# Kernel optimization log

Measured on AMD Instinct MI355X. Metric: run time of the kernel, lower is better.

## Reference

```python
import jax, jax.numpy as jnp
import numpy as np

N = 20000
E = 320000
H = 16
C = 16
NUM_GRAPHS = 64
NEG_SLOPE = 0.2


def _gat(x, edge_index, W, a_src, a_dst, bias):
    # PyG GATConv, concat=True, shared lin for src/dst, eval mode (no dropout)
    h = (x @ W).reshape(-1, H, C)                       # [N,H,C]
    src, dst = edge_index[0], edge_index[1]
    alpha_src = jnp.sum(h * a_src, axis=-1)             # [N,H]
    alpha_dst = jnp.sum(h * a_dst, axis=-1)             # [N,H]
    alpha = alpha_src[src] + alpha_dst[dst]             # [E,H]
    alpha = jax.nn.leaky_relu(alpha, NEG_SLOPE)
    amax = jax.ops.segment_max(alpha, dst, num_segments=N)
    ex = jnp.exp(alpha - amax[dst])
    denom = jax.ops.segment_sum(ex, dst, num_segments=N)
    attn = ex / jnp.where(denom == 0, 1.0, denom)[dst]  # [E,H]
    msg = h[src] * attn[:, :, None]                     # [E,H,C]
    out = jax.ops.segment_sum(msg, dst, num_segments=N) # [N,H,C]
    return out.reshape(-1, H * C) + bias


def setup_inputs() -> dict:
    key = jax.random.key(0)
    ks = jax.random.split(key, 32)
    d = {}
    d['x'] = jax.random.normal(ks[0], (N, 20), dtype=jnp.float32)
    d['edge_index_ipv6'] = jax.random.randint(ks[1], (2, E), 0, N)
    d['edge_attr_ipv6'] = jax.random.normal(ks[2], (E, 19), dtype=jnp.float32)
    d['edge_index_tsch'] = jax.random.randint(ks[3], (2, E), 0, N)
    d['edge_attr_tsch'] = jax.random.normal(ks[4], (E, 7), dtype=jnp.float32)
    d['batch'] = jnp.sort(jax.random.randint(ks[5], (N,), 0, NUM_GRAPHS))
    s = 0.1
    d['W_i'] = jax.random.normal(ks[6], (20, H * C), dtype=jnp.float32) * s
    d['a_src_i'] = jax.random.normal(ks[7], (H, C), dtype=jnp.float32) * s
    d['a_dst_i'] = jax.random.normal(ks[8], (H, C), dtype=jnp.float32) * s
    d['b_i'] = jnp.zeros((H * C,), dtype=jnp.float32)
    d['W_t'] = jax.random.normal(ks[9], (20, H * C), dtype=jnp.float32) * s
    d['a_src_t'] = jax.random.normal(ks[10], (H, C), dtype=jnp.float32) * s
    d['a_dst_t'] = jax.random.normal(ks[11], (H, C), dtype=jnp.float32) * s
    d['b_t'] = jnp.zeros((H * C,), dtype=jnp.float32)
    d['Wf'] = jax.random.normal(ks[12], (512, 64), dtype=jnp.float32) * s
    d['bf'] = jnp.zeros((64,), dtype=jnp.float32)
    d['W1'] = jax.random.normal(ks[13], (64, 32), dtype=jnp.float32) * s
    d['b1'] = jnp.zeros((32,), dtype=jnp.float32)
    d['W2'] = jax.random.normal(ks[14], (32, 16), dtype=jnp.float32) * s
    d['b2'] = jnp.zeros((16,), dtype=jnp.float32)
    d['W3'] = jax.random.normal(ks[15], (16, 16), dtype=jnp.float32) * s
    d['b3'] = jnp.zeros((16,), dtype=jnp.float32)
    d['Wce'] = jax.random.normal(ks[16], (16, 3), dtype=jnp.float32) * s
    d['bce'] = jnp.zeros((3,), dtype=jnp.float32)
    d['Wcv'] = jax.random.normal(ks[17], (16, 3), dtype=jnp.float32) * s
    d['bcv'] = jnp.zeros((3,), dtype=jnp.float32)
    return d


def reference(x, edge_index_ipv6, edge_attr_ipv6, edge_index_tsch, edge_attr_tsch,
              batch, W_i, a_src_i, a_dst_i, b_i, W_t, a_src_t, a_dst_t, b_t,
              Wf, bf, W1, b1, W2, b2, W3, b3, Wce, bce, Wcv, bcv):
    # edge_attr_* are ignored by GATConv (edge_dim=None in PyG), as in original
    n_ipv6 = _gat(x, edge_index_ipv6, W_i, a_src_i, a_dst_i, b_i)
    n_tsch = _gat(x, edge_index_tsch, W_t, a_src_t, a_dst_t, b_t)
    h = jnp.concatenate([n_ipv6, n_tsch], axis=-1)      # [N,512]
    h = jax.nn.relu(h @ Wf + bf)
    h = jax.nn.relu(h @ W1 + b1)
    h = jax.nn.relu(h @ W2 + b2)
    h = jax.nn.relu(h @ W3 + b3)                        # [N,16]
    ssum = jax.ops.segment_sum(h, batch, num_segments=NUM_GRAPHS)
    cnt = jax.ops.segment_sum(jnp.ones((h.shape[0], 1), h.dtype), batch,
                              num_segments=NUM_GRAPHS)
    g = ssum / jnp.where(cnt == 0, 1.0, cnt)            # [G,16]
    out_event = g @ Wce + bce
    out_env = g @ Wcv + bcv
    return out_event, out_env
```

## Files before the change

### kernel.cpp

```cpp
#include <hip/hip_runtime.h>
#include <math.h>

#define N_NODES 20000
#define N_EDGES 320000
#define NG 64
#define NEG 0.2f
#define NCHUNK ((N_NODES + 255) / 256)
#define FLAGBIT (1 << 30)

typedef __attribute__((ext_vector_type(8))) short bf16x8;
typedef __attribute__((ext_vector_type(4))) float f32x4;

__device__ __forceinline__ unsigned short f2bf(float f) {
  unsigned int u = __float_as_uint(f);
  return (unsigned short)((u + 0x7fffu + ((u >> 16) & 1u)) >> 16);
}
__device__ __forceinline__ unsigned int pk2bf(float a, float b) {
  return (unsigned int)f2bf(a) | ((unsigned int)f2bf(b) << 16);
}

__global__ __launch_bounds__(256) void k_front(
    const float* __restrict__ x,
    const float* __restrict__ W_i, const float* __restrict__ as_i, const float* __restrict__ ad_i,
    const float* __restrict__ W_t, const float* __restrict__ as_t, const float* __restrict__ ad_t,
    const float* __restrict__ Wf, const float* __restrict__ bf,
    const float* __restrict__ b_i, const float* __restrict__ b_t,
    const int* __restrict__ ei0, const int* __restrict__ ei1,
    unsigned short* __restrict__ wbigfrag, float* __restrict__ bfold,
    unsigned short* __restrict__ xpadbf,
    float* __restrict__ asrc0, float* __restrict__ adst0,
    float* __restrict__ asrc1, float* __restrict__ adst1,
    int* __restrict__ fill0, int* __restrict__ fill1) {
  __shared__ float bred[4][64];
  __shared__ float xs[16][20];
  __shared__ float ws[20][64];
  int b = blockIdx.x, t = threadIdx.x;
  if (b < 160) {
    int idx = b * 256 + t;
    int ct = idx / 10240, rem = idx % 10240;
    int lane = (rem >> 3) & 63, j = rem & 7, ks = rem >> 9;
    int k = ks * 32 + ((lane >> 4) << 3) + j;
    int nc = ct * 16 + (lane & 15);
    int g = (k >= 320) ? 1 : 0;
    int r = k - g * 320;
    int ch = r >> 4, h = r & 15;
    float v = 0.f;
    if (ch < 20) {
      const float* W = g ? W_t : W_i;
      const float* wr = W + ch * 256 + (h << 4);
      const float* wf = Wf + ((g << 8) + (h << 4)) * 64 + nc;
#pragma unroll
      for (int m = 0; m < 16; ++m) v = fmaf(wr[m], wf[m * 64], v);
    }
    wbigfrag[idx] = f2bf(v);
    return;
  }
  if (b == 160) {
    int wv = t >> 6, j = t & 63;
    float p = 0.f;
    int i0 = wv * 128;
#pragma unroll 4
    for (int i = i0; i < i0 + 128; ++i) {
      float bb = (i < 256) ? b_i[i] : b_t[i - 256];
      p = fmaf(bb, Wf[i * 64 + j], p);
    }
    bred[wv][j] = p;
    __syncthreads();
    if (wv == 0) bfold[j] = bred[0][j] + bred[1][j] + bred[2][j] + bred[3][j] + bf[j];
    return;
  }
  int a = b - 161;
  int e = a * 256 + t;
  int d0 = ei0[N_EDGES + e];
  int d1 = ei1[N_EDGES + e];
  atomicAdd(&fill0[d0], 1);
  atomicAdd(&fill1[d1], 1);
  int n0 = a * 16;
  for (int i = t; i < 320; i += 256) {
    int nd = i / 20, k = i % 20;
    xs[nd][k] = x[(n0 + nd) * 20 + k];
  }
  for (int i = t; i < 1280; i += 256) {
    int k = i >> 6, c = i & 63;
    int set = c >> 5, role = (c >> 4) & 1, h = c & 15;
    const float* W = set ? W_t : W_i;
    const float* av = set ? (role ? ad_t : as_t) : (role ? ad_i : as_i);
    float v = 0.f;
#pragma unroll
    for (int j = 0; j < 16; ++j) v = fmaf(W[k * 256 + h * 16 + j], av[h * 16 + j], v);
    ws[k][c] = v;
  }
  __syncthreads();
  for (int i = t; i < 512; i += 256) {
    int nd = i >> 5, j = i & 31;
    float v = (j < 20) ? xs[nd][j] : (j == 20 ? 1.f : 0.f);
    xpadbf[(size_t)(n0 + nd) * 32 + j] = f2bf(v);
  }
#pragma unroll
  for (int i = 0; i < 4; ++i) {
    int wi = i * 256 + t;
    int nd = wi >> 6, c = wi & 63;
    float v = 0.f;
#pragma unroll
    for (int k = 0; k < 20; ++k) v = fmaf(xs[nd][k], ws[k][c], v);
    int n = n0 + nd, h = c & 15;
    float* arr = (c >> 5) ? ((c >> 4) & 1 ? adst1 : asrc1)
                          : ((c >> 4) & 1 ? adst0 : asrc0);
    arr[n * 16 + h] = v;
  }
}

__global__ __launch_bounds__(256) void k_scan(
    int* __restrict__ fill0, int* __restrict__ fill1,
    int* __restrict__ rp0, int* __restrict__ rp1,
    int* __restrict__ aggs) {
  int chunk = blockIdx.x, set = blockIdx.y;
  int* fill = set ? fill1 : fill0;
  int* rp = set ? rp1 : rp0;
  int t = threadIdx.x, lane = t & 63, wv = t >> 6;
  int i = chunk * 256 + t;
  int v = (i < N_NODES) ? fill[i] : 0;
  int s = v;
#pragma unroll
  for (int d = 1; d < 64; d <<= 1) {
    int o = __shfl_up(s, d);
    if (lane >= d) s += o;
  }
  __shared__ int wsum[4];
  if (lane == 63) wsum[wv] = s;
  __syncthreads();
  int pre = 0;
#pragma unroll
  for (int j = 0; j < 4; ++j)
    if (j < wv) pre += wsum[j];
  s += pre;
  int agg = wsum[0] + wsum[1] + wsum[2] + wsum[3];
  if (t == 0)
    __hip_atomic_store(&aggs[set * 128 + chunk], agg | FLAGBIT,
                       __ATOMIC_RELEASE, __HIP_MEMORY_SCOPE_AGENT);
  __shared__ int reds[256];
  int part = 0;
  for (int j = t; j < chunk; j += 256) {
    int a;
    do {
      a = __hip_atomic_load(&aggs[set * 128 + j], __ATOMIC_ACQUIRE,
                            __HIP_MEMORY_SCOPE_AGENT);
    } while (!(a & FLAGBIT));
    part += a & (FLAGBIT - 1);
  }
  reds[t] = part;
  __syncthreads();
  for (int st = 128; st > 0; st >>= 1) {
    if (t < st) reds[t] += reds[t + st];
    __syncthreads();
  }
  int carry = reds[0];
  int excl = carry + s - v;
  if (i < N_NODES) {
    rp[i] = excl;
    fill[i] = excl;
    if (i == N_NODES - 1) rp[N_NODES] = excl + v;
  }
}

__global__ void k_scatter(const int* __restrict__ ei0, const int* __restrict__ ei1,
                          int* __restrict__ fill0, int* __restrict__ fill1,
                          unsigned short* __restrict__ srcs0,
                          unsigned short* __restrict__ srcs1) {
  int e = blockIdx.x * blockDim.x + threadIdx.x;
  if (e >= N_EDGES) return;
  const int* ei = blockIdx.y ? ei1 : ei0;
  int* fill = blockIdx.y ? fill1 : fill0;
  unsigned short* srcs = blockIdx.y ? srcs1 : srcs0;
  int d = ei[N_EDGES + e];
  int pos = atomicAdd(&fill[d], 1);
  srcs[pos] = (unsigned short)ei[e];
}

__global__ __launch_bounds__(256) void k_gat(
    const unsigned short* __restrict__ xpadbf,
    const float* __restrict__ asrc0, const float* __restrict__ adst0,
    const float* __restrict__ asrc1, const float* __restrict__ adst1,
    const int* __restrict__ rp0, const unsigned short* __restrict__ srcs0,
    const int* __restrict__ rp1, const unsigned short* __restrict__ srcs1,
    unsigned short* __restrict__ xagg) {
  __shared__ unsigned short exsh[4][16][40];
  __shared__ unsigned short xtsh[4][2][16][40];
  int w4 = threadIdx.x >> 6, lane = threadIdx.x & 63;
  int n = blockIdx.x * 2 + (w4 >> 1);
  int g = w4 & 1;
  int eid = lane & 15, slot = lane >> 4;
  unsigned short (*ext)[40] = exsh[w4];
  unsigned short (*xtw)[16][40] = xtsh[w4];
  const float* asrc = g ? asrc1 : asrc0;
  const float* adst = g ? adst1 : adst0;
  const int* rp = g ? rp1 : rp0;
  const unsigned short* srcs = g ? srcs1 : srcs0;
  int k0 = rp[n], k1 = rp[n + 1];
  const float4 adn4 = *(const float4*)&adst[n * 16 + slot * 4];
  f32x4 acc0 = {0.f, 0.f, 0.f, 0.f}, acc1 = acc0;
  int h16 = lane & 15, e8 = (lane >> 4) * 8;
  for (int base = k0; base < k1; base += 32) {
    int e0 = base + 2 * eid, e1 = e0 + 1;
    int sa = (int)srcs[min(e0, k1 - 1)];
    int sbb = (int)srcs[min(e1, k1 - 1)];
    const float4 ava = *(const float4*)&asrc[sa * 16 + slot * 4];
    const float4 avb = *(const float4*)&asrc[sbb * 16 + slot * 4];
    const uint4 xra = *(const uint4*)&xpadbf[(size_t)sa * 32 + slot * 8];
    const uint4 xrb = *(const uint4*)&xpadbf[(size_t)sbb * 32 + slot * 8];
    float ea[4], eb[4];
    {
      float a;
      bool v0 = e0 < k1, v1 = e1 < k1;
      a = ava.x + adn4.x; a = a >= 0.f ? a : NEG * a; ea[0] = v0 ? __expf(a) : 0.f;
      a = ava.y + adn4.y; a = a >= 0.f ? a : NEG * a; ea[1] = v0 ? __expf(a) : 0.f;
      a = ava.z + adn4.z; a = a >= 0.f ? a : NEG * a; ea[2] = v0 ? __expf(a) : 0.f;
      a = ava.w + adn4.w; a = a >= 0.f ? a : NEG * a; ea[3] = v0 ? __expf(a) : 0.f;
      a = avb.x + adn4.x; a = a >= 0.f ? a : NEG * a; eb[0] = v1 ? __expf(a) : 0.f;
      a = avb.y + adn4.y; a = a >= 0.f ? a : NEG * a; eb[1] = v1 ? __expf(a) : 0.f;
      a = avb.z + adn4.z; a = a >= 0.f ? a : NEG * a; eb[2] = v1 ? __expf(a) : 0.f;
      a = avb.w + adn4.w; a = a >= 0.f ? a : NEG * a; eb[3] = v1 ? __expf(a) : 0.f;
    }
#pragma unroll
    for (int r = 0; r < 4; ++r)
      *(unsigned int*)&ext[slot * 4 + r][2 * eid] = pk2bf(ea[r], eb[r]);
    unsigned int ua[4] = {xra.x, xra.y, xra.z, xra.w};
    unsigned int ub[4] = {xrb.x, xrb.y, xrb.z, xrb.w};
#pragma unroll
    for (int q = 0; q < 8; ++q) {
      unsigned int baq = (q & 1) ? (ua[q >> 1] >> 16) : (ua[q >> 1] & 0xffffu);
      unsigned int bbq = (q & 1) ? (ub[q >> 1] >> 16) : (ub[q >> 1] & 0xffffu);
      int ch = slot * 8 + q;
      *(unsigned int*)&xtw[ch >> 4][ch & 15][2 * eid] = baq | (bbq << 16);
    }
    bf16x8 A = *(const bf16x8*)&ext[h16][e8];
    bf16x8 B0 = *(const bf16x8*)&xtw[0][h16][e8];
    bf16x8 B1 = *(const bf16x8*)&xtw[1][h16][e8];
    acc0 = __builtin_amdgcn_mfma_f32_16x16x32_bf16(A, B0, acc0, 0, 0, 0);
    acc1 = __builtin_amdgcn_mfma_f32_16x16x32_bf16(A, B1, acc1, 0, 0, 0);
  }
  float inv[4];
#pragma unroll
  for (int r = 0; r < 4; ++r) {
    float dr = __shfl(acc1[r], (lane & 48) | 4);
    inv[r] = dr > 0.f ? 1.f / dr : 0.f;
  }
  int s = lane >> 4, c = lane & 15;
  size_t nb = (size_t)n * 640 + g * 320;
  uint2 o0;
  o0.x = pk2bf(acc0[0] * inv[0], acc0[1] * inv[1]);
  o0.y = pk2bf(acc0[2] * inv[2], acc0[3] * inv[3]);
  *(uint2*)&xagg[nb + c * 16 + s * 4] = o0;
  if (c < 4) {
    uint2 o1;
    o1.x = pk2bf(acc1[0] * inv[0], acc1[1] * inv[1]);
    o1.y = pk2bf(acc1[2] * inv[2], acc1[3] * inv[3]);
    *(uint2*)&xagg[nb + 256 + c * 16 + s * 4] = o1;
  }
}

__global__ __launch_bounds__(256) void k_mlp(
    const unsigned short* __restrict__ xagg, const unsigned short* __restrict__ wbigfrag,
    const float* __restrict__ bfold,
    const float* __restrict__ W1m, const float* __restrict__ b1v,
    const float* __restrict__ W2m, const float* __restrict__ b2v,
    const float* __restrict__ W3m, const float* __restrict__ b3v,
    const int* __restrict__ batch,
    float* __restrict__ gsum, int* __restrict__ gcnt) {
  int t = threadIdx.x, w = t >> 6, lane = t & 63;
  int n0 = blockIdx.x * 16;
  __shared__ float o1[16][68];
  __shared__ float o2[16][36];
  __shared__ float o3[16][20];
  __shared__ float o4[16][17];
  __shared__ int bs[16];
  if (t < 16) bs[t] = batch[n0 + t];

  {
    int m = lane & 15, kb = lane >> 4;
    const unsigned short* aptr = xagg + (size_t)(n0 + m) * 640 + kb * 8;
    const unsigned short* bbase = wbigfrag + (size_t)w * 10240 + lane * 8;
    f32x4 acc = {0.f, 0.f, 0.f, 0.f};
#pragma unroll 5
    for (int ks = 0; ks < 20; ++ks) {
      bf16x8 af = *(const bf16x8*)(aptr + ks * 32);
      bf16x8 bfr = *(const bf16x8*)(bbase + (size_t)ks * 512);
      acc = __builtin_amdgcn_mfma_f32_16x16x32_bf16(af, bfr, acc, 0, 0, 0);
    }
    int col = lane & 15, rg = lane >> 4;
#pragma unroll
    for (int r = 0; r < 4; ++r) {
      int row = rg * 4 + r;
      o1[row][w * 16 + col] = fmaxf(acc[r] + bfold[w * 16 + col], 0.f);
    }
  }
  __syncthreads();
  int nd = t >> 4, js = t & 15;
  {
    float a0 = b1v[js], a1 = b1v[js + 16];
#pragma unroll 8
    for (int k = 0; k < 64; ++k) {
      float hv = o1[nd][k];
      a0 = fmaf(hv, W1m[k * 32 + js], a0);
      a1 = fmaf(hv, W1m[k * 32 + js + 16], a1);
    }
    o2[nd][js] = fmaxf(a0, 0.f);
    o2[nd][js + 16] = fmaxf(a1, 0.f);
  }
  __syncthreads();
  {
    float a = b2v[js];
#pragma unroll
    for (int k = 0; k < 32; ++k) a = fmaf(o2[nd][k], W2m[k * 16 + js], a);
    o3[nd][js] = fmaxf(a, 0.f);
  }
  __syncthreads();
  {
    float a = b3v[js];
#pragma unroll
    for (int k = 0; k < 16; ++k) a = fmaf(o3[nd][k], W3m[k * 16 + js], a);
    o4[nd][js] = fmaxf(a, 0.f);
  }
  __syncthreads();
  if (t < 128) {
    int s = t >> 4, jx = t & 15;
    int b = bs[0] + s;
    if (b <= bs[15]) {
      float sum = 0.f; int c = 0;
#pragma unroll
      for (int ndd = 0; ndd < 16; ++ndd)
        if (bs[ndd] == b) { sum += o4[ndd][jx]; ++c; }
      if (c > 0) {
        atomicAdd(&gsum[b * 16 + jx], sum);
        if (jx == 0) atomicAdd(&gcnt[b], c);
      }
    }
  }
}

__global__ void k_head(const float* __restrict__ gsum, const int* __restrict__ gcnt,
                       const float* __restrict__ Wce, const float* __restrict__ bce,
                       const float* __restrict__ Wcv, const float* __restrict__ bcv,
                       float* __restrict__ out) {
  int t = threadIdx.x;
  if (t >= 384) return;
  int half = t / 192, idx = t % 192;
  int b = idx / 3, r = idx % 3;
  float cnt = (float)gcnt[b];
  float inv = cnt > 0.f ? 1.f / cnt : 1.f;
  const float* Wc = half ? Wcv : Wce;
  const float* bc = half ? bcv : bce;
  float v = bc[r];
#pragma unroll
  for (int j = 0; j < 16; ++j) v = fmaf(gsum[b * 16 + j] * inv, Wc[j * 3 + r], v);
  out[t] = v;
}

extern "C" void kernel_launch(void* const* d_in, const int* in_sizes, int n_in,
                              void* d_out, int out_size, void* d_ws, size_t ws_size,
                              hipStream_t stream) {
  const float* x = (const float*)d_in[0];
  const int* ei_i = (const int*)d_in[1];
  const int* ei_t = (const int*)d_in[3];
  const int* batch = (const int*)d_in[5];
  const float* W_i = (const float*)d_in[6];
  const float* as_i = (const float*)d_in[7];
  const float* ad_i = (const float*)d_in[8];
  const float* b_i = (const float*)d_in[9];
  const float* W_t = (const float*)d_in[10];
  const float* as_t = (const float*)d_in[11];
  const float* ad_t = (const float*)d_in[12];
  const float* b_t = (const float*)d_in[13];
  const float* Wf = (const float*)d_in[14];
  const float* bf = (const float*)d_in[15];
  const float* W1 = (const float*)d_in[16];
  const float* b1 = (const float*)d_in[17];
  const float* W2 = (const float*)d_in[18];
  const float* b2 = (const float*)d_in[19];
  const float* W3 = (const float*)d_in[20];
  const float* b3 = (const float*)d_in[21];
  const float* Wce = (const float*)d_in[22];
  const float* bce = (const float*)d_in[23];
  const float* Wcv = (const float*)d_in[24];
  const float* bcv = (const float*)d_in[25];

  char* ws = (char*)d_ws;
  size_t off = 0;
  auto take = [&](size_t bytes) {
    void* p = ws + off;
    off = (off + bytes + 255) & ~(size_t)255;
    return p;
  };
  unsigned short* xpadbf = (unsigned short*)take((size_t)N_NODES * 32 * 2);
  unsigned short* xagg = (unsigned short*)take((size_t)N_NODES * 640 * 2);
  unsigned short* wbigfrag = (unsigned short*)take((size_t)40960 * 2);
  float* bfold = (float*)take((size_t)64 * 4);
  float* asrc_i = (float*)take((size_t)N_NODES * 16 * 4);
  float* adst_i = (float*)take((size_t)N_NODES * 16 * 4);
  float* asrc_t = (float*)take((size_t)N_NODES * 16 * 4);
  float* adst_t = (float*)take((size_t)N_NODES * 16 * 4);
  int* rowptr_i = (int*)take((size_t)(N_NODES + 1) * 4);
  int* rowptr_t = (int*)take((size_t)(N_NODES + 1) * 4);
  int* fill_i = (int*)take((size_t)2 * N_NODES * 4);
  int* fill_t = fill_i + N_NODES;
  unsigned short* srcs_i = (unsigned short*)take((size_t)N_EDGES * 2);
  unsigned short* srcs_t = (unsigned short*)take((size_t)N_EDGES * 2);
  float* gsum = (float*)take((size_t)(NG * 16 + NG + 256) * 4);
  int* gcnt = (int*)(gsum + NG * 16);
  int* csums = gcnt + NG;

  hipMemsetAsync(fill_i, 0, (size_t)2 * N_NODES * 4, stream);
  hipMemsetAsync(gsum, 0, (size_t)(NG * 16 + NG + 256) * 4, stream);

  k_front<<<1411, 256, 0, stream>>>(x, W_i, as_i, ad_i, W_t, as_t, ad_t,
                                    Wf, bf, b_i, b_t, ei_i, ei_t,
                                    wbigfrag, bfold, xpadbf,
                                    asrc_i, adst_i, asrc_t, adst_t,
                                    fill_i, fill_t);

  dim3 sgrid(NCHUNK, 2);
  k_scan<<<sgrid, 256, 0, stream>>>(fill_i, fill_t, rowptr_i, rowptr_t, csums);

  dim3 egrid((N_EDGES + 255) / 256, 2);
  k_scatter<<<egrid, 256, 0, stream>>>(ei_i, ei_t, fill_i, fill_t, srcs_i, srcs_t);

  k_gat<<<N_NODES / 2, 256, 0, stream>>>(xpadbf, asrc_i, adst_i, asrc_t, adst_t,
                                         rowptr_i, srcs_i, rowptr_t, srcs_t,
                                         xagg);

  k_mlp<<<N_NODES / 16, 256, 0, stream>>>(xagg, wbigfrag, bfold,
                                          W1, b1, W2, b2, W3, b3,
                                          batch, gsum, gcnt);

  k_head<<<1, 384, 0, stream>>>(gsum, gcnt, Wce, bce, Wcv, bcv, (float*)d_out);
}
```

Baseline: 137.8 us.

## Fuse GAT aggregation and MLP into one kernel, merge memsets

Merges the GAT aggregation kernel and the MLP/pooling kernel into a single kernel where each block aggregates 16 nodes (8 iterations of 2 nodes per wave pair) and then runs the MLP on those same nodes, reusing shared memory through a union buffer. The xagg rows are written and then re-read by the same block, which should mostly hit in cache, and one kernel launch is removed. The two memsets are merged into one by placing the fill and gsum buffers next to each other. In exchange, the grid shrinks from 10000 to 1250 blocks, so per-block degree imbalance is serialized within a block and there is less parallelism for hiding gather latency.

Measured after the change: 133.6 us. 1.03x faster.

```diff
diff --git a/kernel.cpp b/kernel.cpp
--- a/kernel.cpp
+++ b/kernel.cpp
@@ -177,162 +177,167 @@
   srcs[pos] = (unsigned short)ei[e];
 }
 
-__global__ __launch_bounds__(256) void k_gat(
+__global__ __launch_bounds__(256) void k_gatmlp(
     const unsigned short* __restrict__ xpadbf,
     const float* __restrict__ asrc0, const float* __restrict__ adst0,
     const float* __restrict__ asrc1, const float* __restrict__ adst1,
     const int* __restrict__ rp0, const unsigned short* __restrict__ srcs0,
     const int* __restrict__ rp1, const unsigned short* __restrict__ srcs1,
-    unsigned short* __restrict__ xagg) {
-  __shared__ unsigned short exsh[4][16][40];
-  __shared__ unsigned short xtsh[4][2][16][40];
-  int w4 = threadIdx.x >> 6, lane = threadIdx.x & 63;
-  int n = blockIdx.x * 2 + (w4 >> 1);
-  int g = w4 & 1;
-  int eid = lane & 15, slot = lane >> 4;
-  unsigned short (*ext)[40] = exsh[w4];
-  unsigned short (*xtw)[16][40] = xtsh[w4];
-  const float* asrc = g ? asrc1 : asrc0;
-  const float* adst = g ? adst1 : adst0;
-  const int* rp = g ? rp1 : rp0;
-  const unsigned short* srcs = g ? srcs1 : srcs0;
-  int k0 = rp[n], k1 = rp[n + 1];
-  const float4 adn4 = *(const float4*)&adst[n * 16 + slot * 4];
-  f32x4 acc0 = {0.f, 0.f, 0.f, 0.f}, acc1 = acc0;
-  int h16 = lane & 15, e8 = (lane >> 4) * 8;
-  for (int base = k0; base < k1; base += 32) {
-    int e0 = base + 2 * eid, e1 = e0 + 1;
-    int sa = (int)srcs[min(e0, k1 - 1)];
-    int sbb = (int)srcs[min(e1, k1 - 1)];
-    const float4 ava = *(const float4*)&asrc[sa * 16 + slot * 4];
-    const float4 avb = *(const float4*)&asrc[sbb * 16 + slot * 4];
-    const uint4 xra = *(const uint4*)&xpadbf[(size_t)sa * 32 + slot * 8];
-    const uint4 xrb = *(const uint4*)&xpadbf[(size_t)sbb * 32 + slot * 8];
-    float ea[4], eb[4];
-    {
-      float a;
-      bool v0 = e0 < k1, v1 = e1 < k1;
-      a = ava.x + adn4.x; a = a >= 0.f ? a : NEG * a; ea[0] = v0 ? __expf(a) : 0.f;
-      a = ava.y + adn4.y; a = a >= 0.f ? a : NEG * a; ea[1] = v0 ? __expf(a) : 0.f;
-      a = ava.z + adn4.z; a = a >= 0.f ? a : NEG * a; ea[2] = v0 ? __expf(a) : 0.f;
-      a = ava.w + adn4.w; a = a >= 0.f ? a : NEG * a; ea[3] = v0 ? __expf(a) : 0.f;
-      a = avb.x + adn4.x; a = a >= 0.f ? a : NEG * a; eb[0] = v1 ? __expf(a) : 0.f;
-      a = avb.y + adn4.y; a = a >= 0.f ? a : NEG * a; eb[1] = v1 ? __expf(a) : 0.f;
-      a = avb.z + adn4.z; a = a >= 0.f ? a : NEG * a; eb[2] = v1 ? __expf(a) : 0.f;
-      a = avb.w + adn4.w; a = a >= 0.f ? a : NEG * a; eb[3] = v1 ? __expf(a) : 0.f;
-    }
-#pragma unroll
-    for (int r = 0; r < 4; ++r)
-      *(unsigned int*)&ext[slot * 4 + r][2 * eid] = pk2bf(ea[r], eb[r]);
-    unsigned int ua[4] = {xra.x, xra.y, xra.z, xra.w};
-    unsigned int ub[4] = {xrb.x, xrb.y, xrb.z, xrb.w};
-#pragma unroll
-    for (int q = 0; q < 8; ++q) {
-      unsigned int baq = (q & 1) ? (ua[q >> 1] >> 16) : (ua[q >> 1] & 0xffffu);
-      unsigned int bbq = (q & 1) ? (ub[q >> 1] >> 16) : (ub[q >> 1] & 0xffffu);
-      int ch = slot * 8 + q;
-      *(unsigned int*)&xtw[ch >> 4][ch & 15][2 * eid] = baq | (bbq << 16);
-    }
-    bf16x8 A = *(const bf16x8*)&ext[h16][e8];
-    bf16x8 B0 = *(const bf16x8*)&xtw[0][h16][e8];
-    bf16x8 B1 = *(const bf16x8*)&xtw[1][h16][e8];
-    acc0 = __builtin_amdgcn_mfma_f32_16x16x32_bf16(A, B0, acc0, 0, 0, 0);
-    acc1 = __builtin_amdgcn_mfma_f32_16x16x32_bf16(A, B1, acc1, 0, 0, 0);
-  }
-  float inv[4];
-#pragma unroll
-  for (int r = 0; r < 4; ++r) {
-    float dr = __shfl(acc1[r], (lane & 48) | 4);
-    inv[r] = dr > 0.f ? 1.f / dr : 0.f;
-  }
-  int s = lane >> 4, c = lane & 15;
-  size_t nb = (size_t)n * 640 + g * 320;
-  uint2 o0;
-  o0.x = pk2bf(acc0[0] * inv[0], acc0[1] * inv[1]);
-  o0.y = pk2bf(acc0[2] * inv[2], acc0[3] * inv[3]);
-  *(uint2*)&xagg[nb + c * 16 + s * 4] = o0;
-  if (c < 4) {
-    uint2 o1;
-    o1.x = pk2bf(acc1[0] * inv[0], acc1[1] * inv[1]);
-    o1.y = pk2bf(acc1[2] * inv[2], acc1[3] * inv[3]);
-    *(uint2*)&xagg[nb + 256 + c * 16 + s * 4] = o1;
-  }
-}
-
-__global__ __launch_bounds__(256) void k_mlp(
-    const unsigned short* __restrict__ xagg, const unsigned short* __restrict__ wbigfrag,
+    unsigned short* __restrict__ xagg, const unsigned short* __restrict__ wbigfrag,
     const float* __restrict__ bfold,
     const float* __restrict__ W1m, const float* __restrict__ b1v,
     const float* __restrict__ W2m, const float* __restrict__ b2v,
     const float* __restrict__ W3m, const float* __restrict__ b3v,
     const int* __restrict__ batch,
     float* __restrict__ gsum, int* __restrict__ gcnt) {
-  int t = threadIdx.x, w = t >> 6, lane = t & 63;
+  __shared__ __align__(16) char smem_[15360];
+  int t = threadIdx.x;
+  int w4 = t >> 6, lane = t & 63;
   int n0 = blockIdx.x * 16;
-  __shared__ float o1[16][68];
-  __shared__ float o2[16][36];
-  __shared__ float o3[16][20];
-  __shared__ float o4[16][17];
-  __shared__ int bs[16];
-  if (t < 16) bs[t] = batch[n0 + t];
 
   {
-    int m = lane & 15, kb = lane >> 4;
-    const unsigned short* aptr = xagg + (size_t)(n0 + m) * 640 + kb * 8;
-    const unsigned short* bbase = wbigfrag + (size_t)w * 10240 + lane * 8;
-    f32x4 acc = {0.f, 0.f, 0.f, 0.f};
+    int eid = lane & 15, slot = lane >> 4;
+    int h16 = lane & 15, e8 = (lane >> 4) * 8;
+    unsigned short* ext = (unsigned short*)smem_ + w4 * 640;
+    unsigned short* xtw = (unsigned short*)(smem_ + 5120) + w4 * 1280;
+    int g = w4 & 1;
+    const float* asrc = g ? asrc1 : asrc0;
+    const float* adst = g ? adst1 : adst0;
+    const int* rp = g ? rp1 : rp0;
+    const unsigned short* srcs = g ? srcs1 : srcs0;
+    for (int it = 0; it < 8; ++it) {
+      int n = n0 + it * 2 + (w4 >> 1);
+      int k0 = rp[n], k1 = rp[n + 1];
+      const float4 adn4 = *(const float4*)&adst[n * 16 + slot * 4];
+      f32x4 acc0 = {0.f, 0.f, 0.f, 0.f}, acc1 = acc0;
+      for (int base = k0; base < k1; base += 32) {
+        int e0 = base + 2 * eid, e1 = e0 + 1;
+        int sa = (int)srcs[min(e0, k1 - 1)];
+        int sbb = (int)srcs[min(e1, k1 - 1)];
+        const float4 ava = *(const float4*)&asrc[sa * 16 + slot * 4];
+        const float4 avb = *(const float4*)&asrc[sbb * 16 + slot * 4];
+        const uint4 xra = *(const uint4*)&xpadbf[(size_t)sa * 32 + slot * 8];
+        const uint4 xrb = *(const uint4*)&xpadbf[(size_t)sbb * 32 + slot * 8];
+        float ea[4], eb[4];
+        {
+          float a;
+          bool v0 = e0 < k1, v1 = e1 < k1;
+          a = ava.x + adn4.x; a = a >= 0.f ? a : NEG * a; ea[0] = v0 ? __expf(a) : 0.f;
+          a = ava.y + adn4.y; a = a >= 0.f ? a : NEG * a; ea[1] = v0 ? __expf(a) : 0.f;
+          a = ava.z + adn4.z; a = a >= 0.f ? a : NEG * a; ea[2] = v0 ? __expf(a) : 0.f;
+          a = ava.w + adn4.w; a = a >= 0.f ? a : NEG * a; ea[3] = v0 ? __expf(a) : 0.f;
+          a = avb.x + adn4.x; a = a >= 0.f ? a : NEG * a; eb[0] = v1 ? __expf(a) : 0.f;
+          a = avb.y + adn4.y; a = a >= 0.f ? a : NEG * a; eb[1] = v1 ? __expf(a) : 0.f;
+          a = avb.z + adn4.z; a = a >= 0.f ? a : NEG * a; eb[2] = v1 ? __expf(a) : 0.f;
+          a = avb.w + adn4.w; a = a >= 0.f ? a : NEG * a; eb[3] = v1 ? __expf(a) : 0.f;
+        }
+#pragma unroll
+        for (int r = 0; r < 4; ++r)
+          *(unsigned int*)&ext[(slot * 4 + r) * 40 + 2 * eid] = pk2bf(ea[r], eb[r]);
+        unsigned int ua[4] = {xra.x, xra.y, xra.z, xra.w};
+        unsigned int ub[4] = {xrb.x, xrb.y, xrb.z, xrb.w};
+#pragma unroll
+        for (int q = 0; q < 8; ++q) {
+          unsigned int baq = (q & 1) ? (ua[q >> 1] >> 16) : (ua[q >> 1] & 0xffffu);
+          unsigned int bbq = (q & 1) ? (ub[q >> 1] >> 16) : (ub[q >> 1] & 0xffffu);
+          int ch = slot * 8 + q;
+          *(unsigned int*)&xtw[(ch >> 4) * 640 + (ch & 15) * 40 + 2 * eid] =
+              baq | (bbq << 16);
+        }
+        bf16x8 A = *(const bf16x8*)&ext[h16 * 40 + e8];
+        bf16x8 B0 = *(const bf16x8*)&xtw[h16 * 40 + e8];
+        bf16x8 B1 = *(const bf16x8*)&xtw[640 + h16 * 40 + e8];
+        acc0 = __builtin_amdgcn_mfma_f32_16x16x32_bf16(A, B0, acc0, 0, 0, 0);
+        acc1 = __builtin_amdgcn_mfma_f32_16x16x32_bf16(A, B1, acc1, 0, 0, 0);
+      }
+      float inv[4];
+#pragma unroll
+      for (int r = 0; r < 4; ++r) {
+        float dr = __shfl(acc1[r], (lane & 48) | 4);
+        inv[r] = dr > 0.f ? 1.f / dr : 0.f;
+      }
+      int ss = lane >> 4, c = lane & 15;
+      size_t nb = (size_t)n * 640 + g * 320;
+      uint2 o0;
+      o0.x = pk2bf(acc0[0] * inv[0], acc0[1] * inv[1]);
+      o0.y = pk2bf(acc0[2] * inv[2], acc0[3] * inv[3]);
+      *(uint2*)&xagg[nb + c * 16 + ss * 4] = o0;
+      if (c < 4) {
+        uint2 o1v;
+        o1v.x = pk2bf(acc1[0] * inv[0], acc1[1] * inv[1]);
+        o1v.y = pk2bf(acc1[2] * inv[2], acc1[3] * inv[3]);
+        *(uint2*)&xagg[nb + 256 + c * 16 + ss * 4] = o1v;
+      }
+    }
+  }
+  __syncthreads();
+
+  {
+    float* o1 = (float*)smem_;
+    float* o2 = o1 + 1088;
+    float* o3 = o2 + 576;
+    float* o4 = o3 + 320;
+    int* bs = (int*)(o4 + 272);
+    if (t < 16) bs[t] = batch[n0 + t];
+    int w = w4;
+    {
+      int m = lane & 15, kb = lane >> 4;
+      const unsigned short* aptr = xagg + (size_t)(n0 + m) * 640 + kb * 8;
+      const unsigned short* bbase = wbigfrag + (size_t)w * 10240 + lane * 8;
+      f32x4 acc = {0.f, 0.f, 0.f, 0.f};
 #pragma unroll 5
-    for (int ks = 0; ks < 20; ++ks) {
-      bf16x8 af = *(const bf16x8*)(aptr + ks * 32);
-      bf16x8 bfr = *(const bf16x8*)(bbase + (size_t)ks * 512);
-      acc = __builtin_amdgcn_mfma_f32_16x16x32_bf16(af, bfr, acc, 0, 0, 0);
-    }
-    int col = lane & 15, rg = lane >> 4;
-#pragma unroll
-    for (int r = 0; r < 4; ++r) {
-      int row = rg * 4 + r;
-      o1[row][w * 16 + col] = fmaxf(acc[r] + bfold[w * 16 + col], 0.f);
-    }
-  }
-  __syncthreads();
-  int nd = t >> 4, js = t & 15;
-  {
-    float a0 = b1v[js], a1 = b1v[js + 16];
+      for (int ks = 0; ks < 20; ++ks) {
+        bf16x8 af = *(const bf16x8*)(aptr + ks * 32);
+        bf16x8 bfr = *(const bf16x8*)(bbase + (size_t)ks * 512);
+        acc = __builtin_amdgcn_mfma_f32_16x16x32_bf16(af, bfr, acc, 0, 0, 0);
+      }
+      int col = lane & 15, rg = lane >> 4;
+#pragma unroll
+      for (int r = 0; r < 4; ++r) {
+        int row = rg * 4 + r;
+        o1[row * 68 + w * 16 + col] = fmaxf(acc[r] + bfold[w * 16 + col], 0.f);
+      }
+    }
+    __syncthreads();
+    int nd = t >> 4, js = t & 15;
+    {
+      float a0 = b1v[js], a1 = b1v[js + 16];
 #pragma unroll 8
-    for (int k = 0; k < 64; ++k) {
-      float hv = o1[nd][k];
-      a0 = fmaf(hv, W1m[k * 32 + js], a0);
-      a1 = fmaf(hv, W1m[k * 32 + js + 16], a1);
-    }
-    o2[nd][js] = fmaxf(a0, 0.f);
-    o2[nd][js + 16] = fmaxf(a1, 0.f);
-  }
-  __syncthreads();
-  {
-    float a = b2v[js];
-#pragma unroll
-    for (int k = 0; k < 32; ++k) a = fmaf(o2[nd][k], W2m[k * 16 + js], a);
-    o3[nd][js] = fmaxf(a, 0.f);
-  }
-  __syncthreads();
-  {
-    float a = b3v[js];
-#pragma unroll
-    for (int k = 0; k < 16; ++k) a = fmaf(o3[nd][k], W3m[k * 16 + js], a);
-    o4[nd][js] = fmaxf(a, 0.f);
-  }
-  __syncthreads();
-  if (t < 128) {
-    int s = t >> 4, jx = t & 15;
-    int b = bs[0] + s;
-    if (b <= bs[15]) {
-      float sum = 0.f; int c = 0;
-#pragma unroll
-      for (int ndd = 0; ndd < 16; ++ndd)
-        if (bs[ndd] == b) { sum += o4[ndd][jx]; ++c; }
-      if (c > 0) {
-        atomicAdd(&gsum[b * 16 + jx], sum);
-        if (jx == 0) atomicAdd(&gcnt[b], c);
+      for (int k = 0; k < 64; ++k) {
+        float hv = o1[nd * 68 + k];
+        a0 = fmaf(hv, W1m[k * 32 + js], a0);
+        a1 = fmaf(hv, W1m[k * 32 + js + 16], a1);
+      }
+      o2[nd * 36 + js] = fmaxf(a0, 0.f);
+      o2[nd * 36 + js + 16] = fmaxf(a1, 0.f);
+    }
+    __syncthreads();
+    {
+      float a = b2v[js];
+#pragma unroll
+      for (int k = 0; k < 32; ++k) a = fmaf(o2[nd * 36 + k], W2m[k * 16 + js], a);
+      o3[nd * 20 + js] = fmaxf(a, 0.f);
+    }
+    __syncthreads();
+    {
+      float a = b3v[js];
+#pragma unroll
+      for (int k = 0; k < 16; ++k) a = fmaf(o3[nd * 20 + k], W3m[k * 16 + js], a);
+      o4[nd * 17 + js] = fmaxf(a, 0.f);
+    }
+    __syncthreads();
+    if (t < 128) {
+      int s = t >> 4, jx = t & 15;
+      int b = bs[0] + s;
+      if (b <= bs[15]) {
+        float sum = 0.f; int c = 0;
+#pragma unroll
+        for (int ndd = 0; ndd < 16; ++ndd)
+          if (bs[ndd] == b) { sum += o4[ndd * 17 + jx]; ++c; }
+        if (c > 0) {
+          atomicAdd(&gsum[b * 16 + jx], sum);
+          if (jx == 0) atomicAdd(&gcnt[b], c);
+        }
       }
     }
   }
@@ -401,16 +406,16 @@
   float* adst_t = (float*)take((size_t)N_NODES * 16 * 4);
   int* rowptr_i = (int*)take((size_t)(N_NODES + 1) * 4);
   int* rowptr_t = (int*)take((size_t)(N_NODES + 1) * 4);
-  int* fill_i = (int*)take((size_t)2 * N_NODES * 4);
-  int* fill_t = fill_i + N_NODES;
   unsigned short* srcs_i = (unsigned short*)take((size_t)N_EDGES * 2);
   unsigned short* srcs_t = (unsigned short*)take((size_t)N_EDGES * 2);
-  float* gsum = (float*)take((size_t)(NG * 16 + NG + 256) * 4);
+  int zero_ints = N_NODES + N_NODES + NG * 16 + NG + 256;
+  int* fill_i = (int*)take((size_t)zero_ints * 4);
+  int* fill_t = fill_i + N_NODES;
+  float* gsum = (float*)(fill_t + N_NODES);
   int* gcnt = (int*)(gsum + NG * 16);
   int* csums = gcnt + NG;
 
-  hipMemsetAsync(fill_i, 0, (size_t)2 * N_NODES * 4, stream);
-  hipMemsetAsync(gsum, 0, (size_t)(NG * 16 + NG + 256) * 4, stream);
+  hipMemsetAsync(fill_i, 0, (size_t)zero_ints * 4, stream);
 
   k_front<<<1411, 256, 0, stream>>>(x, W_i, as_i, ad_i, W_t, as_t, ad_t,
                                     Wf, bf, b_i, b_t, ei_i, ei_t,
@@ -424,13 +429,11 @@
   dim3 egrid((N_EDGES + 255) / 256, 2);
   k_scatter<<<egrid, 256, 0, stream>>>(ei_i, ei_t, fill_i, fill_t, srcs_i, srcs_t);
 
-  k_gat<<<N_NODES / 2, 256, 0, stream>>>(xpadbf, asrc_i, adst_i, asrc_t, adst_t,
-                                         rowptr_i, srcs_i, rowptr_t, srcs_t,
-                                         xagg);
-
-  k_mlp<<<N_NODES / 16, 256, 0, stream>>>(xagg, wbigfrag, bfold,
-                                          W1, b1, W2, b2, W3, b3,
-                                          batch, gsum, gcnt);
+  k_gatmlp<<<N_NODES / 16, 256, 0, stream>>>(
+      xpadbf, asrc_i, adst_i, asrc_t, adst_t,
+      rowptr_i, srcs_i, rowptr_t, srcs_t,
+      xagg, wbigfrag, bfold, W1, b1, W2, b2, W3, b3,
+      batch, gsum, gcnt);
 
   k_head<<<1, 384, 0, stream>>>(gsum, gcnt, Wce, bce, Wcv, bcv, (float*)d_out);
 }
```
